# Optimization experiments

Measured on AMD Instinct MI355X. Metric: run time of the kernel, lower is better.

## Reference

```python
import jax, jax.numpy as jnp
import numpy as np

IN_FEATURES = 4096
RANK = 64
NUM_EXPERTS = 8
ALPHA = 64.0
SPARSITY = 0.8
SCALING = ALPHA / RANK  # alpha / rank


def setup_inputs() -> dict:
    key = jax.random.key(0)
    k1, k2, k3, k4 = jax.random.split(key, 4)
    B, S = 4, 4096
    projected_input = jax.random.normal(k1, (B, S, RANK), dtype=jnp.float32)
    routing_weights = jax.random.uniform(k2, (B, S, NUM_EXPERTS), dtype=jnp.float32)
    # Stacked expert A matrices [K, in_features, rank] (kaiming-like init ~ normal here)
    A = jax.random.normal(k3, (NUM_EXPERTS, IN_FEATURES, RANK), dtype=jnp.float32) * 0.02
    sparse_mask = (jax.random.uniform(k4, (NUM_EXPERTS, IN_FEATURES, RANK)) >= SPARSITY).astype(jnp.float32)
    A = A * sparse_mask  # module masks A at init as well
    return {
        "projected_input": projected_input,
        "routing_weights": routing_weights,
        "A": A,
        "sparse_mask": sparse_mask,
    }


def reference(projected_input, routing_weights, A, sparse_mask):
    # A_sparse[k] = A[k] * mask[k]; per expert: scaling * (p @ A_sparse[k].T)
    # then weighted sum over experts with routing_weights[..., k].
    A_eff = (A * sparse_mask) * SCALING          # [k, d, r]
    # Weight the rank-projected input per expert, then contract:
    # wp[b,s,k,r] = routing_weights[b,s,k] * projected_input[b,s,r]
    wp = jnp.einsum("bsk,bsr->bskr", routing_weights, projected_input)
    out = jnp.einsum("bskr,kdr->bsd", wp, A_eff)  # [b, s, in_features]
    return out
```

## Files before the change

### kernel.cpp

```cpp
#include <hip/hip_runtime.h>

#define IN_FEATURES 4096
#define RANK 64
#define NUM_EXPERTS 8
#define KDIM 512
#define TOKENS 16384
#define SCALING 1.0f

#define BM 256
#define BN 256
#define BK 64
#define NKT (KDIM / BK)
#define NIT (NKT / 2)

typedef __bf16 bf16x8 __attribute__((ext_vector_type(8)));
typedef float f32x4 __attribute__((ext_vector_type(4)));

__device__ __forceinline__ unsigned short f2bf(float f) {
  union { float f; unsigned int u; } v; v.f = f;
  unsigned int u = v.u;
  u += 0x7fffu + ((u >> 16) & 1u);
  return (unsigned short)(u >> 16);
}

__device__ __forceinline__ void gload_lds16(const unsigned short* g, unsigned short* l) {
  __builtin_amdgcn_global_load_lds(
      (const __attribute__((address_space(1))) void*)g,
      (__attribute__((address_space(3))) void*)l,
      16, 0, 0);
}

__global__ void __launch_bounds__(256) q_pack(const float* __restrict__ p,
                                              const float* __restrict__ w,
                                              unsigned short* __restrict__ q) {
  int t = blockIdx.x;
  int i = threadIdx.x;
  int k = i >> 5;
  int rp = (i & 31) * 2;
  float wk = w[t * NUM_EXPERTS + k];
  float p0 = p[t * RANK + rp];
  float p1 = p[t * RANK + rp + 1];
  ushort2 o;
  o.x = f2bf(wk * p0);
  o.y = f2bf(wk * p1);
  *(ushort2*)&q[t * KDIM + k * RANK + rp] = o;
}

__global__ void __launch_bounds__(256) b_pack(const float* __restrict__ A,
                                              const float* __restrict__ mask,
                                              unsigned short* __restrict__ Bt) {
  int d = blockIdx.x;
  int i = threadIdx.x;
  int k = i >> 5;
  int rp = (i & 31) * 2;
  long src = ((long)k * IN_FEATURES + d) * RANK + rp;
  float a0 = A[src] * mask[src] * SCALING;
  float a1 = A[src + 1] * mask[src + 1] * SCALING;
  ushort2 o;
  o.x = f2bf(a0);
  o.y = f2bf(a1);
  *(ushort2*)&Bt[d * KDIM + k * RANK + rp] = o;
}

__global__ void __launch_bounds__(512, 2) gemm_kernel(
    const unsigned short* __restrict__ q,
    const unsigned short* __restrict__ Bt,
    float* __restrict__ out) {
  __shared__ __align__(16) unsigned short sA[2][2][128 * BK];
  __shared__ __align__(16) unsigned short sB[2][2][128 * BK];

  const int tid = threadIdx.x;
  const int lane = tid & 63;
  const int wid = tid >> 6;
  const int u = lane & 15;
  const int quad = lane >> 4;
  const int hA = wid >> 2;
  const int hB = (wid & 3) >> 1;
  const int rB = (wid & 1) * 64;
  const int wn = (wid & 3) * 64;

  const int m0 = blockIdx.y * BM;
  const int n0 = blockIdx.x * BN;

  f32x4 acc[8][4];
#pragma unroll
  for (int i = 0; i < 8; ++i)
#pragma unroll
    for (int j = 0; j < 4; ++j)
      acc[i][j] = (f32x4){0.f, 0.f, 0.f, 0.f};

  const int c0 = tid, c1 = tid + 512;
  const int row0 = c0 >> 3, row1 = c1 >> 3;
  const int log0 = (c0 & 7) ^ (row0 & 7), log1 = (c1 & 7) ^ (row1 & 7);
  const unsigned short* gA0 = q + (m0 + row0) * KDIM + log0 * 8;
  const unsigned short* gA1 = q + (m0 + row1) * KDIM + log1 * 8;
  const unsigned short* gB0 = Bt + (n0 + row0) * KDIM + log0 * 8;
  const unsigned short* gB1 = Bt + (n0 + row1) * KDIM + log1 * 8;
  const int l0 = c0 * 8, l1 = c1 * 8;

  auto stageA = [&](int buf, int h, int kt) {
    int ko = (kt & (NKT - 1)) * BK + h * 128 * KDIM;
    gload_lds16(gA0 + ko, &sA[buf][h][l0]);
    gload_lds16(gA1 + ko, &sA[buf][h][l1]);
  };
  auto stageB = [&](int buf, int h, int kt) {
    int ko = (kt & (NKT - 1)) * BK + h * 128 * KDIM;
    gload_lds16(gB0 + ko, &sB[buf][h][l0]);
    gload_lds16(gB1 + ko, &sB[buf][h][l1]);
  };

  auto ldA = [&](int buf, int mq, bf16x8 (&a)[2][4]) {
    const unsigned short* base = sA[buf][hA];
#pragma unroll
    for (int ki = 0; ki < 2; ++ki)
#pragma unroll
      for (int f = 0; f < 4; ++f) {
        int r = mq * 64 + f * 16 + u;
        int phys = (ki * 4 + quad) ^ (r & 7);
        a[ki][f] = *(const bf16x8*)&base[r * BK + phys * 8];
      }
  };
  auto ldB = [&](int buf, int nq, bf16x8 (&b)[2][2]) {
    const unsigned short* base = sB[buf][hB];
#pragma unroll
    for (int ki = 0; ki < 2; ++ki)
#pragma unroll
      for (int g = 0; g < 2; ++g) {
        int r = rB + nq * 32 + g * 16 + u;
        int phys = (ki * 4 + quad) ^ (r & 7);
        b[ki][g] = *(const bf16x8*)&base[r * BK + phys * 8];
      }
  };
  auto mfmaQ = [&](int mq, int nq, bf16x8 (&a)[2][4], bf16x8 (&b)[2][2]) {
    __builtin_amdgcn_s_setprio(1);
#pragma unroll
    for (int ki = 0; ki < 2; ++ki)
#pragma unroll
      for (int f = 0; f < 4; ++f)
#pragma unroll
        for (int g = 0; g < 2; ++g)
          acc[mq * 4 + f][nq * 2 + g] = __builtin_amdgcn_mfma_f32_16x16x32_bf16(
              a[ki][f], b[ki][g], acc[mq * 4 + f][nq * 2 + g], 0, 0, 0);
    __builtin_amdgcn_s_setprio(0);
  };
  auto phase_bar = [&]() {
    __builtin_amdgcn_sched_barrier(0);
    __builtin_amdgcn_s_barrier();
  };

  bf16x8 Ar[2][4], B0r[2][2], B1r[2][2];

  stageB(0, 0, 0); stageB(0, 1, 0);
  stageA(0, 0, 0); stageA(0, 1, 0);
  stageB(1, 0, 1); stageB(1, 1, 1);
  asm volatile("s_waitcnt vmcnt(4)" ::: "memory");
  phase_bar();

  for (int i = 0; i < NIT; ++i) {
    const int k1 = 2 * i + 1, k2 = 2 * i + 2, k3 = 2 * i + 3;
    ldA(0, 0, Ar); ldB(0, 0, B0r);
    stageA(1, 0, k1);
    phase_bar();
    mfmaQ(0, 0, Ar, B0r);
    phase_bar();
    ldB(0, 1, B1r);
    stageA(1, 1, k1);
    phase_bar();
    mfmaQ(0, 1, Ar, B1r);
    phase_bar();
    ldA(0, 1, Ar);
    stageB(0, 0, k2);
    phase_bar();
    mfmaQ(1, 1, Ar, B1r);
    phase_bar();
    stageB(0, 1, k2);
    phase_bar();
    mfmaQ(1, 0, Ar, B0r);
    asm volatile("s_waitcnt vmcnt(4)" ::: "memory");
    phase_bar();
    ldA(1, 0, Ar); ldB(1, 0, B0r);
    stageA(0, 0, k2);
    phase_bar();
    mfmaQ(0, 0, Ar, B0r);
    phase_bar();
    ldB(1, 1, B1r);
    stageA(0, 1, k2);
    phase_bar();
    mfmaQ(0, 1, Ar, B1r);
    phase_bar();
    ldA(1, 1, Ar);
    stageB(1, 0, k3);
    phase_bar();
    mfmaQ(1, 1, Ar, B1r);
    phase_bar();
    stageB(1, 1, k3);
    phase_bar();
    mfmaQ(1, 0, Ar, B0r);
    asm volatile("s_waitcnt vmcnt(4)" ::: "memory");
    phase_bar();
  }

#pragma unroll
  for (int mf = 0; mf < 8; ++mf) {
    int row = m0 + hA * 128 + mf * 16 + quad * 4;
#pragma unroll
    for (int rr = 0; rr < 4; ++rr) {
      float* orow = out + (long)(row + rr) * IN_FEATURES + n0 + wn + u;
#pragma unroll
      for (int nf = 0; nf < 4; ++nf)
        orow[nf * 16] = acc[mf][nf][rr];
    }
  }
}

extern "C" void kernel_launch(void* const* d_in, const int* in_sizes, int n_in,
                              void* d_out, int out_size, void* d_ws, size_t ws_size,
                              hipStream_t stream) {
  const float* p    = (const float*)d_in[0];
  const float* w    = (const float*)d_in[1];
  const float* A    = (const float*)d_in[2];
  const float* mask = (const float*)d_in[3];
  float* out = (float*)d_out;

  unsigned short* q  = (unsigned short*)d_ws;
  unsigned short* Bt = q + (size_t)TOKENS * KDIM;

  q_pack<<<TOKENS, 256, 0, stream>>>(p, w, q);
  b_pack<<<IN_FEATURES, 256, 0, stream>>>(A, mask, Bt);

  dim3 grid(IN_FEATURES / BN, TOKENS / BM);
  gemm_kernel<<<grid, dim3(512), 0, stream>>>(q, Bt, out);
}
```

Measured before the change: 343.7 us.

## Fuse q and B pack kernels with float4 loads, swap GEMM grid order

Merges the two packing kernels into one launch in which each thread handles four elements through float4 loads and ushort4 stores, cutting one launch and improving memory access width. The GEMM grid is also transposed so that consecutive blocks walk the token dimension while sharing the same B tile, which changes L2 reuse. Index math now uses the flat gid with a branch between the two pack regions.

Measured after the change: 345.3 us. No clear change (+0.5%).

```diff
diff --git a/kernel.cpp b/kernel.cpp
--- a/kernel.cpp
+++ b/kernel.cpp
@@ -30,36 +30,41 @@
       16, 0, 0);
 }
 
-__global__ void __launch_bounds__(256) q_pack(const float* __restrict__ p,
-                                              const float* __restrict__ w,
-                                              unsigned short* __restrict__ q) {
-  int t = blockIdx.x;
-  int i = threadIdx.x;
-  int k = i >> 5;
-  int rp = (i & 31) * 2;
-  float wk = w[t * NUM_EXPERTS + k];
-  float p0 = p[t * RANK + rp];
-  float p1 = p[t * RANK + rp + 1];
-  ushort2 o;
-  o.x = f2bf(wk * p0);
-  o.y = f2bf(wk * p1);
-  *(ushort2*)&q[t * KDIM + k * RANK + rp] = o;
-}
-
-__global__ void __launch_bounds__(256) b_pack(const float* __restrict__ A,
-                                              const float* __restrict__ mask,
-                                              unsigned short* __restrict__ Bt) {
-  int d = blockIdx.x;
-  int i = threadIdx.x;
-  int k = i >> 5;
-  int rp = (i & 31) * 2;
-  long src = ((long)k * IN_FEATURES + d) * RANK + rp;
-  float a0 = A[src] * mask[src] * SCALING;
-  float a1 = A[src + 1] * mask[src + 1] * SCALING;
-  ushort2 o;
-  o.x = f2bf(a0);
-  o.y = f2bf(a1);
-  *(ushort2*)&Bt[d * KDIM + k * RANK + rp] = o;
+#define QN4 ((long)TOKENS * KDIM / 4)
+#define BN4 ((long)IN_FEATURES * KDIM / 4)
+__global__ void __launch_bounds__(256) pack_both(
+    const float* __restrict__ p, const float* __restrict__ w,
+    const float* __restrict__ A, const float* __restrict__ mask,
+    unsigned short* __restrict__ q, unsigned short* __restrict__ Bt) {
+  long gid = (long)blockIdx.x * 256 + threadIdx.x;
+  if (gid < QN4) {
+    int idx = (int)gid;
+    int t = idx >> 7;
+    int k = (idx >> 4) & 7;
+    int r0 = (idx & 15) * 4;
+    float wk = w[t * NUM_EXPERTS + k];
+    float4 pv = *(const float4*)&p[t * RANK + r0];
+    ushort4 o;
+    o.x = f2bf(wk * pv.x);
+    o.y = f2bf(wk * pv.y);
+    o.z = f2bf(wk * pv.z);
+    o.w = f2bf(wk * pv.w);
+    *(ushort4*)&q[(long)t * KDIM + k * RANK + r0] = o;
+  } else {
+    int idx = (int)(gid - QN4);
+    int d = idx >> 7;
+    int k = (idx >> 4) & 7;
+    int r0 = (idx & 15) * 4;
+    long src = ((long)k * IN_FEATURES + d) * RANK + r0;
+    float4 a = *(const float4*)&A[src];
+    float4 m = *(const float4*)&mask[src];
+    ushort4 o;
+    o.x = f2bf(a.x * m.x * SCALING);
+    o.y = f2bf(a.y * m.y * SCALING);
+    o.z = f2bf(a.z * m.z * SCALING);
+    o.w = f2bf(a.w * m.w * SCALING);
+    *(ushort4*)&Bt[(long)d * KDIM + k * RANK + r0] = o;
+  }
 }
 
 __global__ void __launch_bounds__(512, 2) gemm_kernel(
@@ -79,8 +84,8 @@
   const int rB = (wid & 1) * 64;
   const int wn = (wid & 3) * 64;
 
-  const int m0 = blockIdx.y * BM;
-  const int n0 = blockIdx.x * BN;
+  const int m0 = blockIdx.x * BM;
+  const int n0 = blockIdx.y * BN;
 
   f32x4 acc[8][4];
 #pragma unroll
@@ -225,9 +230,9 @@
   unsigned short* q  = (unsigned short*)d_ws;
   unsigned short* Bt = q + (size_t)TOKENS * KDIM;
 
-  q_pack<<<TOKENS, 256, 0, stream>>>(p, w, q);
-  b_pack<<<IN_FEATURES, 256, 0, stream>>>(A, mask, Bt);
-
-  dim3 grid(IN_FEATURES / BN, TOKENS / BM);
+  int pack_blocks = (int)((QN4 + BN4) / 256);
+  pack_both<<<pack_blocks, 256, 0, stream>>>(p, w, A, mask, q, Bt);
+
+  dim3 grid(TOKENS / BM, IN_FEATURES / BN);
   gemm_kernel<<<grid, dim3(512), 0, stream>>>(q, Bt, out);
 }
```
